# Performance work log

Measured on AMD Instinct MI355X. Metric: run time of the kernel, lower is better.

## Reference

```python
import jax, jax.numpy as jnp
import numpy as np

B, H, L, D = 8, 8, 2048, 64
FACTOR = 5


def _num_sel(length):
    return min(int(FACTOR * np.ceil(np.log(length))), length)


def setup_inputs() -> dict:
    key = jax.random.key(0)
    kq, kk, kv, ki = jax.random.split(key, 4)
    num_k = _num_sel(L)
    return {
        "q": jax.random.normal(kq, (B, H, L, D), dtype=jnp.float32),
        "k": jax.random.normal(kk, (B, H, L, D), dtype=jnp.float32),
        "v": jax.random.normal(kv, (B, H, L, D), dtype=jnp.float32),
        "random_index": jax.random.randint(ki, (L, num_k), 0, L, dtype=jnp.int32),
    }


def reference(q, k, v, random_index):
    b, h, q_len, d = q.shape
    k_len = k.shape[2]
    num_q = _num_sel(q_len)

    # --- random K sampling per query: k_s[b,h,i,j,:] = k[b,h,random_index[i,j],:]
    k_s = k[:, :, random_index, :]                      # (B,H,L,num_k,D)
    pre_attn = jnp.einsum('bhid,bhijd->bhij', q, k_s)   # (B,H,L,num_k)
    measure = pre_attn.max(-1) - pre_attn.sum(-1) / k_len  # (B,H,L)

    # --- top-k query selection (sorted=False in torch; order-insensitive math)
    _, idx = jax.lax.top_k(measure, num_q)              # (B,H,num_q)
    q_sel = jnp.take_along_axis(q, idx[..., None], axis=2)  # (B,H,num_q,D)

    # --- reduced attention over all keys
    attn = jnp.einsum('bhid,bhjd->bhij', q_sel, k) * (d ** -0.5)  # (B,H,num_q,k_len)

    # ProbMask: causal mask per selected query index (mask where j > idx[i])
    mask = jnp.arange(k_len)[None, None, None, :] > idx[..., None]
    attn = jnp.where(mask, -jnp.inf, attn)
    attn = jax.nn.softmax(attn, axis=-1)

    out_sel = jnp.einsum('bhij,bhjd->bhid', attn, v)    # (B,H,num_q,D)

    # --- context initialization (use_mask=True branch) and scatter back
    context = jnp.cumsum(v, axis=2)                     # (B,H,L,D)
    bi = jnp.arange(b)[:, None, None]
    hi = jnp.arange(h)[None, :, None]
    out = context.at[bi, hi, idx].set(out_sel)          # (B,H,L,D)
    return out, attn
```

## Files before the change

### kernel.cpp

```cpp
#include <hip/hip_runtime.h>
#include <float.h>
#include <math.h>

#define B_  8
#define H_  8
#define L_  2048
#define D_  64
#define NS  40
#define BH  (B_*H_)
#define SCALE 0.125f


__global__ __launch_bounds__(256) void measure_kernel(
    const float* __restrict__ q, const float* __restrict__ k,
    const int* __restrict__ ridx, float* __restrict__ measure)
{
    int wave = threadIdx.x >> 6, lane = threadIdx.x & 63;
    int b = blockIdx.x;
    int xcd = b & 7, s = b >> 3;
    int bh  = xcd + ((s >> 9) << 3);
    int i   = (s & 511) * 4 + wave;
    int qj  = lane >> 4;
    int d4  = lane & 15;

    int rs = ridx[i * NS + (lane < NS ? lane : NS - 1)];

    const float4* kb = (const float4*)(k + (size_t)bh * L_ * D_);
    float4 qq = ((const float4*)(q + ((size_t)bh * L_ + i) * D_))[d4];

    float mx = -FLT_MAX, sm = 0.f;
    #pragma unroll
    for (int p = 0; p < 10; ++p) {
        int j = p * 4 + qj;
        int r = __shfl(rs, j, 64);
        float4 kk = kb[(size_t)r * 16 + d4];
        float pp = qq.x*kk.x + qq.y*kk.y + qq.z*kk.z + qq.w*kk.w;
        pp += __shfl_xor(pp, 1, 64);
        pp += __shfl_xor(pp, 2, 64);
        pp += __shfl_xor(pp, 4, 64);
        pp += __shfl_xor(pp, 8, 64);
        mx = fmaxf(mx, pp);
        sm += pp;
    }
    mx = fmaxf(mx, __shfl_xor(mx, 16, 64));  sm += __shfl_xor(sm, 16, 64);
    mx = fmaxf(mx, __shfl_xor(mx, 32, 64));  sm += __shfl_xor(sm, 32, 64);
    if (lane == 0)
        measure[(size_t)bh * L_ + i] = mx - sm * (1.0f / (float)L_);
}

__global__ __launch_bounds__(256) void topk_kernel(
    const float* __restrict__ measure, int* __restrict__ idxOut)
{
    __shared__ float wv[4]; __shared__ int wi[4];
    __shared__ float bvS;   __shared__ int biS;
    int b = blockIdx.x;
    int bh = (b & 7) + ((b >> 3) << 3);
    int t = threadIdx.x;
    const float4* m4 = (const float4*)(measure + (size_t)bh * L_);
    float vals[8];
    float4 a = m4[t*2], bb = m4[t*2 + 1];
    vals[0]=a.x; vals[1]=a.y; vals[2]=a.z; vals[3]=a.w;
    vals[4]=bb.x; vals[5]=bb.y; vals[6]=bb.z; vals[7]=bb.w;

    float lv = -FLT_MAX; int li = t*8;
    #pragma unroll
    for (int e = 0; e < 8; ++e) if (vals[e] > lv) { lv = vals[e]; li = t*8 + e; }

    int lane = t & 63, w = t >> 6;
    for (int r = 0; r < NS; ++r) {
        float v = lv; int idx = li;
        #pragma unroll
        for (int off = 32; off; off >>= 1) {
            float ov = __shfl_xor(v, off, 64);
            int   oi = __shfl_xor(idx, off, 64);
            if (ov > v || (ov == v && oi < idx)) { v = ov; idx = oi; }
        }
        if (lane == 0) { wv[w] = v; wi[w] = idx; }
        __syncthreads();
        if (t == 0) {
            float bv = wv[0]; int bi = wi[0];
            #pragma unroll
            for (int ww = 1; ww < 4; ++ww)
                if (wv[ww] > bv || (wv[ww] == bv && wi[ww] < bi)) { bv = wv[ww]; bi = wi[ww]; }
            bvS = bv; biS = bi;
            idxOut[bh * NS + r] = bi;
        }
        __syncthreads();
        int bi = biS;
        if ((bi >> 3) == t) {
            #pragma unroll
            for (int e = 0; e < 8; ++e) if ((bi & 7) == e) vals[e] = -FLT_MAX;
            lv = -FLT_MAX; li = t*8;
            #pragma unroll
            for (int e = 0; e < 8; ++e) if (vals[e] > lv) { lv = vals[e]; li = t*8 + e; }
        }
        __syncthreads();
    }
}

__global__ __launch_bounds__(256) void cumsum_p1(
    const float* __restrict__ v, float4* __restrict__ vpart)
{
    __shared__ float4 part[16][16];
    int b = blockIdx.x;
    int xcd = b & 7, s = b >> 3;
    int bh = xcd + ((s >> 4) << 3);
    int c  = s & 15;
    int d4 = threadIdx.x & 15, sub = threadIdx.x >> 4;
    const float4* vb = (const float4*)(v + (size_t)bh * L_ * D_);
    int r0 = c*128 + sub*8;
    float4 acc = make_float4(0,0,0,0);
    #pragma unroll
    for (int r = 0; r < 8; ++r) {
        float4 x = vb[(r0 + r)*16 + d4];
        acc.x += x.x; acc.y += x.y; acc.z += x.z; acc.w += x.w;
    }
    part[sub][d4] = acc;
    __syncthreads();
    if (sub == 0) {
        float4 tot = part[0][d4];
        #pragma unroll
        for (int ss = 1; ss < 16; ++ss) {
            float4 x = part[ss][d4];
            tot.x += x.x; tot.y += x.y; tot.z += x.z; tot.w += x.w;
        }
        vpart[(bh*16 + c)*16 + d4] = tot;
    }
}

__global__ __launch_bounds__(256) void cumsum_p2(
    const float* __restrict__ v, const float4* __restrict__ vpart,
    float* __restrict__ out)
{
    __shared__ float4 part[16][16];
    int b = blockIdx.x;
    int xcd = b & 7, s = b >> 3;
    int bh = xcd + ((s >> 4) << 3);
    int c  = s & 15;
    int d4 = threadIdx.x & 15, sub = threadIdx.x >> 4;
    const float4* vb = (const float4*)(v + (size_t)bh * L_ * D_);
    float4*       ob = (float4*)(out + (size_t)bh * L_ * D_);
    int r0 = c*128 + sub*8;
    float4 acc = make_float4(0,0,0,0);
    #pragma unroll
    for (int r = 0; r < 8; ++r) {
        float4 x = vb[(r0 + r)*16 + d4];
        acc.x += x.x; acc.y += x.y; acc.z += x.z; acc.w += x.w;
    }
    part[sub][d4] = acc;
    float4 run = make_float4(0,0,0,0);
    for (int cc = 0; cc < c; ++cc) {
        float4 x = vpart[(bh*16 + cc)*16 + d4];
        run.x += x.x; run.y += x.y; run.z += x.z; run.w += x.w;
    }
    __syncthreads();
    #pragma unroll
    for (int ss = 0; ss < 16; ++ss) {
        if (ss < sub) {
            float4 x = part[ss][d4];
            run.x += x.x; run.y += x.y; run.z += x.z; run.w += x.w;
        }
    }
    #pragma unroll
    for (int r = 0; r < 8; ++r) {
        float4 x = vb[(r0 + r)*16 + d4];
        run.x += x.x; run.y += x.y; run.z += x.z; run.w += x.w;
        ob[(r0 + r)*16 + d4] = run;
    }
}

__global__ __launch_bounds__(256) void scores_kernel(
    const float* __restrict__ q, const float* __restrict__ k,
    const int* __restrict__ idxSel, float* __restrict__ attn)
{
    __shared__ float4 kbuf[16 * 129];
    int b = blockIdx.x;
    int xcd = b & 7, s = b >> 3;
    int bh  = xcd + ((s / 10) << 3);
    int grp = s % 10;
    int qi = threadIdx.x >> 6, sub = threadIdx.x & 63;
    int rank = grp*4 + qi;
    int qrow = idxSel[bh*NS + rank];

    const float4* qrp = (const float4*)(q + ((size_t)bh * L_ + qrow) * D_);
    float4 qreg[16];
    #pragma unroll
    for (int g = 0; g < 16; ++g) qreg[g] = qrp[g];

    const float4* kb = (const float4*)(k + (size_t)bh * L_ * D_);
    float sc0[16], sc1[16];

    #pragma unroll
    for (int c = 0; c < 16; ++c) {
        __syncthreads();
        int j0 = c * 128;
        #pragma unroll
        for (int it = 0; it < 8; ++it) {
            int fi = threadIdx.x + 256*it;
            int g = fi & 15, j = fi >> 4;
            kbuf[g*129 + j] = kb[(size_t)(j0 + j)*16 + g];
        }
        __syncthreads();
        float acc0 = 0.f, acc1 = 0.f;
        #pragma unroll
        for (int g = 0; g < 16; ++g) {
            float4 k0 = kbuf[g*129 + sub];
            float4 k1 = kbuf[g*129 + sub + 64];
            float4 qq = qreg[g];
            acc0 += qq.x*k0.x + qq.y*k0.y + qq.z*k0.z + qq.w*k0.w;
            acc1 += qq.x*k1.x + qq.y*k1.y + qq.z*k1.z + qq.w*k1.w;
        }
        sc0[c] = acc0 * SCALE;
        sc1[c] = acc1 * SCALE;
    }

    float mx = -FLT_MAX;
    #pragma unroll
    for (int c = 0; c < 16; ++c) {
        if (c*128 + sub      <= qrow) mx = fmaxf(mx, sc0[c]);
        if (c*128 + sub + 64 <= qrow) mx = fmaxf(mx, sc1[c]);
    }
    #pragma unroll
    for (int off = 32; off; off >>= 1) mx = fmaxf(mx, __shfl_xor(mx, off, 64));

    float sum = 0.f;
    #pragma unroll
    for (int c = 0; c < 16; ++c) {
        sc0[c] = (c*128 + sub      <= qrow) ? __expf(sc0[c] - mx) : 0.f;
        sc1[c] = (c*128 + sub + 64 <= qrow) ? __expf(sc1[c] - mx) : 0.f;
        sum += sc0[c] + sc1[c];
    }
    #pragma unroll
    for (int off = 32; off; off >>= 1) sum += __shfl_xor(sum, off, 64);
    float inv = 1.f / sum;

    float* arow = attn + (size_t)(bh*NS + rank) * L_;
    #pragma unroll
    for (int c = 0; c < 16; ++c) {
        arow[c*128 + sub]      = sc0[c] * inv;
        arow[c*128 + sub + 64] = sc1[c] * inv;
    }
}

__global__ __launch_bounds__(256) void pv_kernel(
    const float* __restrict__ v, const int* __restrict__ idxSel,
    const float* __restrict__ attn, float* __restrict__ out)
{
    __shared__ float wl[4][L_ + 64];
    __shared__ float4 part[16][16];
    __shared__ int qr4[4];
    int b = blockIdx.x;
    int xcd = b & 7, s = b >> 3;
    int bh  = xcd + ((s / 10) << 3);
    int grp = s % 10;
    int t = threadIdx.x;
    if (t < 4) qr4[t] = idxSel[bh*NS + grp*4 + t];

    #pragma unroll
    for (int it = 0; it < 8; ++it) {
        int f = t + 256*it;
        int rr = f >> 9, fi = f & 511;
        const float4* ar = (const float4*)(attn + (size_t)(bh*NS + grp*4 + rr) * L_);
        float4 x = ar[fi];
        int j = 4*fi;
        *((float4*)&wl[rr][j + 4*(j >> 7)]) = x;
    }
    __syncthreads();

    int maxq = max(max(qr4[0], qr4[1]), max(qr4[2], qr4[3]));
    int d4 = t & 15, seg = t >> 4;
    const float4* vb = (const float4*)(v + (size_t)bh * L_ * D_);
    float4 acc[4];
    #pragma unroll
    for (int rr = 0; rr < 4; ++rr) acc[rr] = make_float4(0,0,0,0);

    int jlo = seg*128, jhi = min(jlo + 127, maxq);
    for (int j = jlo; j <= jhi; ++j) {
        float4 x = vb[(size_t)j*16 + d4];
        int jp = j + 4*(j >> 7);
        #pragma unroll
        for (int rr = 0; rr < 4; ++rr) {
            float wgt = wl[rr][jp];
            acc[rr].x += wgt*x.x; acc[rr].y += wgt*x.y;
            acc[rr].z += wgt*x.z; acc[rr].w += wgt*x.w;
        }
    }

    #pragma unroll
    for (int rr = 0; rr < 4; ++rr) {
        part[seg][d4] = acc[rr];
        __syncthreads();
        float4 a = acc[rr];
        for (int s2 = 8; s2; s2 >>= 1) {
            if (seg < s2) {
                float4 o = part[seg + s2][d4];
                a.x += o.x; a.y += o.y; a.z += o.z; a.w += o.w;
                part[seg][d4] = a;
            }
            __syncthreads();
        }
        if (seg == 0) {
            float4* orow = (float4*)(out + ((size_t)bh * L_ + qr4[rr]) * D_);
            orow[d4] = a;
        }
        __syncthreads();
    }
}

extern "C" void kernel_launch(void* const* d_in, const int* in_sizes, int n_in,
                              void* d_out, int out_size, void* d_ws, size_t ws_size,
                              hipStream_t stream) {
    const float* q    = (const float*)d_in[0];
    const float* k    = (const float*)d_in[1];
    const float* v    = (const float*)d_in[2];
    const int*   ridx = (const int*)d_in[3];

    float* out     = (float*)d_out;
    float* attnOut = out + (size_t)BH * L_ * D_;

    float*  measure = (float*)d_ws;
    int*    idxSel  = (int*)((char*)d_ws + (size_t)BH * L_ * sizeof(float));
    float4* vpart   = (float4*)d_ws;

    measure_kernel<<<BH * L_ / 4, 256, 0, stream>>>(q, k, ridx, measure);
    topk_kernel   <<<BH,          256, 0, stream>>>(measure, idxSel);
    cumsum_p1     <<<BH * 16,     256, 0, stream>>>(v, vpart);
    cumsum_p2     <<<BH * 16,     256, 0, stream>>>(v, vpart, out);
    scores_kernel <<<BH * 10,     256, 0, stream>>>(q, k, idxSel, attnOut);
    pv_kernel     <<<BH * 10,     256, 0, stream>>>(v, idxSel, attnOut, out);
}
```

Measured before the change: 331.2 us.

## Merge six launches into three fused kernels with DPP reductions

Runs measure together with the cumsum partial pass in one launch, and top-k together with the cumsum final pass in a second. Scores and PV are fused so attention weights go straight into shared memory instead of being reloaded from global. The measure reduction now uses DPP moves in place of shuffles, and random indices are read directly rather than broadcast. Fewer launch gaps and less global traffic, but the fused scores/PV kernel uses more shared memory, which may lower occupancy.

```diff
diff --git a/kernel.cpp b/kernel.cpp
--- a/kernel.cpp
+++ b/kernel.cpp
@@ -11,169 +11,173 @@
 #define SCALE 0.125f
 
 
-__global__ __launch_bounds__(256) void measure_kernel(
+template<int CTRL>
+__device__ __forceinline__ float dpp_mov(float x) {
+    return __int_as_float(__builtin_amdgcn_update_dpp(
+        0, __float_as_int(x), CTRL, 0xf, 0xf, true));
+}
+
+__global__ __launch_bounds__(256) void kernelA(
     const float* __restrict__ q, const float* __restrict__ k,
-    const int* __restrict__ ridx, float* __restrict__ measure)
+    const int* __restrict__ ridx, const float* __restrict__ v,
+    float* __restrict__ measure, float4* __restrict__ vpart)
 {
-    int wave = threadIdx.x >> 6, lane = threadIdx.x & 63;
-    int b = blockIdx.x;
-    int xcd = b & 7, s = b >> 3;
-    int bh  = xcd + ((s >> 9) << 3);
-    int i   = (s & 511) * 4 + wave;
-    int qj  = lane >> 4;
-    int d4  = lane & 15;
-
-    int rs = ridx[i * NS + (lane < NS ? lane : NS - 1)];
-
-    const float4* kb = (const float4*)(k + (size_t)bh * L_ * D_);
-    float4 qq = ((const float4*)(q + ((size_t)bh * L_ + i) * D_))[d4];
-
-    float mx = -FLT_MAX, sm = 0.f;
-    #pragma unroll
-    for (int p = 0; p < 10; ++p) {
-        int j = p * 4 + qj;
-        int r = __shfl(rs, j, 64);
-        float4 kk = kb[(size_t)r * 16 + d4];
-        float pp = qq.x*kk.x + qq.y*kk.y + qq.z*kk.z + qq.w*kk.w;
-        pp += __shfl_xor(pp, 1, 64);
-        pp += __shfl_xor(pp, 2, 64);
-        pp += __shfl_xor(pp, 4, 64);
-        pp += __shfl_xor(pp, 8, 64);
-        mx = fmaxf(mx, pp);
-        sm += pp;
-    }
-    mx = fmaxf(mx, __shfl_xor(mx, 16, 64));  sm += __shfl_xor(sm, 16, 64);
-    mx = fmaxf(mx, __shfl_xor(mx, 32, 64));  sm += __shfl_xor(sm, 32, 64);
-    if (lane == 0)
-        measure[(size_t)bh * L_ + i] = mx - sm * (1.0f / (float)L_);
-}
-
-__global__ __launch_bounds__(256) void topk_kernel(
-    const float* __restrict__ measure, int* __restrict__ idxOut)
-{
-    __shared__ float wv[4]; __shared__ int wi[4];
-    __shared__ float bvS;   __shared__ int biS;
-    int b = blockIdx.x;
-    int bh = (b & 7) + ((b >> 3) << 3);
-    int t = threadIdx.x;
-    const float4* m4 = (const float4*)(measure + (size_t)bh * L_);
-    float vals[8];
-    float4 a = m4[t*2], bb = m4[t*2 + 1];
-    vals[0]=a.x; vals[1]=a.y; vals[2]=a.z; vals[3]=a.w;
-    vals[4]=bb.x; vals[5]=bb.y; vals[6]=bb.z; vals[7]=bb.w;
-
-    float lv = -FLT_MAX; int li = t*8;
-    #pragma unroll
-    for (int e = 0; e < 8; ++e) if (vals[e] > lv) { lv = vals[e]; li = t*8 + e; }
-
-    int lane = t & 63, w = t >> 6;
-    for (int r = 0; r < NS; ++r) {
-        float v = lv; int idx = li;
-        #pragma unroll
-        for (int off = 32; off; off >>= 1) {
-            float ov = __shfl_xor(v, off, 64);
-            int   oi = __shfl_xor(idx, off, 64);
-            if (ov > v || (ov == v && oi < idx)) { v = ov; idx = oi; }
-        }
-        if (lane == 0) { wv[w] = v; wi[w] = idx; }
-        __syncthreads();
-        if (t == 0) {
-            float bv = wv[0]; int bi = wi[0];
+    if (blockIdx.x < 32768) {
+        int wave = threadIdx.x >> 6, lane = threadIdx.x & 63;
+        int b = blockIdx.x;
+        int xcd = b & 7, s = b >> 3;
+        int bh  = xcd + ((s >> 9) << 3);
+        int i   = (s & 511) * 4 + wave;
+        int qj  = lane >> 4;
+        int d4  = lane & 15;
+
+        const float4* kb = (const float4*)(k + (size_t)bh * L_ * D_);
+        float4 qq = ((const float4*)(q + ((size_t)bh * L_ + i) * D_))[d4];
+        const int* rip = ridx + i * NS + qj;
+
+        float mx = -FLT_MAX, sm = 0.f;
+        #pragma unroll
+        for (int p = 0; p < 10; ++p) {
+            int r = rip[p * 4];
+            float4 kk = kb[(size_t)r * 16 + d4];
+            float pp = qq.x*kk.x + qq.y*kk.y + qq.z*kk.z + qq.w*kk.w;
+            pp += dpp_mov<0xB1>(pp);
+            pp += dpp_mov<0x4E>(pp);
+            pp += dpp_mov<0x124>(pp);
+            pp += dpp_mov<0x128>(pp);
+            mx = fmaxf(mx, pp);
+            sm += pp;
+        }
+        mx = fmaxf(mx, dpp_mov<0x142>(mx));  sm += dpp_mov<0x142>(sm);
+        mx = fmaxf(mx, dpp_mov<0x143>(mx));  sm += dpp_mov<0x143>(sm);
+        if (lane == 63)
+            measure[(size_t)bh * L_ + i] = mx - sm * (1.0f / (float)L_);
+    } else {
+        __shared__ float4 part[16][16];
+        int b = blockIdx.x - 32768;
+        int xcd = b & 7, s = b >> 3;
+        int bh = xcd + ((s >> 4) << 3);
+        int c  = s & 15;
+        int d4 = threadIdx.x & 15, sub = threadIdx.x >> 4;
+        const float4* vb = (const float4*)(v + (size_t)bh * L_ * D_);
+        int r0 = c*128 + sub*8;
+        float4 acc = make_float4(0,0,0,0);
+        #pragma unroll
+        for (int r = 0; r < 8; ++r) {
+            float4 x = vb[(r0 + r)*16 + d4];
+            acc.x += x.x; acc.y += x.y; acc.z += x.z; acc.w += x.w;
+        }
+        part[sub][d4] = acc;
+        __syncthreads();
+        if (sub == 0) {
+            float4 tot = part[0][d4];
             #pragma unroll
-            for (int ww = 1; ww < 4; ++ww)
-                if (wv[ww] > bv || (wv[ww] == bv && wi[ww] < bi)) { bv = wv[ww]; bi = wi[ww]; }
-            bvS = bv; biS = bi;
-            idxOut[bh * NS + r] = bi;
-        }
-        __syncthreads();
-        int bi = biS;
-        if ((bi >> 3) == t) {
-            #pragma unroll
-            for (int e = 0; e < 8; ++e) if ((bi & 7) == e) vals[e] = -FLT_MAX;
-            lv = -FLT_MAX; li = t*8;
-            #pragma unroll
-            for (int e = 0; e < 8; ++e) if (vals[e] > lv) { lv = vals[e]; li = t*8 + e; }
-        }
-        __syncthreads();
-    }
-}
-
-__global__ __launch_bounds__(256) void cumsum_p1(
-    const float* __restrict__ v, float4* __restrict__ vpart)
-{
-    __shared__ float4 part[16][16];
-    int b = blockIdx.x;
-    int xcd = b & 7, s = b >> 3;
-    int bh = xcd + ((s >> 4) << 3);
-    int c  = s & 15;
-    int d4 = threadIdx.x & 15, sub = threadIdx.x >> 4;
-    const float4* vb = (const float4*)(v + (size_t)bh * L_ * D_);
-    int r0 = c*128 + sub*8;
-    float4 acc = make_float4(0,0,0,0);
-    #pragma unroll
-    for (int r = 0; r < 8; ++r) {
-        float4 x = vb[(r0 + r)*16 + d4];
-        acc.x += x.x; acc.y += x.y; acc.z += x.z; acc.w += x.w;
-    }
-    part[sub][d4] = acc;
-    __syncthreads();
-    if (sub == 0) {
-        float4 tot = part[0][d4];
-        #pragma unroll
-        for (int ss = 1; ss < 16; ++ss) {
-            float4 x = part[ss][d4];
-            tot.x += x.x; tot.y += x.y; tot.z += x.z; tot.w += x.w;
-        }
-        vpart[(bh*16 + c)*16 + d4] = tot;
-    }
-}
-
-__global__ __launch_bounds__(256) void cumsum_p2(
-    const float* __restrict__ v, const float4* __restrict__ vpart,
+            for (int ss = 1; ss < 16; ++ss) {
+                float4 x = part[ss][d4];
+                tot.x += x.x; tot.y += x.y; tot.z += x.z; tot.w += x.w;
+            }
+            vpart[(bh*16 + c)*16 + d4] = tot;
+        }
+    }
+}
+
+__global__ __launch_bounds__(256) void kernelB(
+    const float* __restrict__ measure, const float* __restrict__ v,
+    const float4* __restrict__ vpart, int* __restrict__ idxOut,
     float* __restrict__ out)
 {
-    __shared__ float4 part[16][16];
-    int b = blockIdx.x;
-    int xcd = b & 7, s = b >> 3;
-    int bh = xcd + ((s >> 4) << 3);
-    int c  = s & 15;
-    int d4 = threadIdx.x & 15, sub = threadIdx.x >> 4;
-    const float4* vb = (const float4*)(v + (size_t)bh * L_ * D_);
-    float4*       ob = (float4*)(out + (size_t)bh * L_ * D_);
-    int r0 = c*128 + sub*8;
-    float4 acc = make_float4(0,0,0,0);
-    #pragma unroll
-    for (int r = 0; r < 8; ++r) {
-        float4 x = vb[(r0 + r)*16 + d4];
-        acc.x += x.x; acc.y += x.y; acc.z += x.z; acc.w += x.w;
-    }
-    part[sub][d4] = acc;
-    float4 run = make_float4(0,0,0,0);
-    for (int cc = 0; cc < c; ++cc) {
-        float4 x = vpart[(bh*16 + cc)*16 + d4];
-        run.x += x.x; run.y += x.y; run.z += x.z; run.w += x.w;
-    }
-    __syncthreads();
-    #pragma unroll
-    for (int ss = 0; ss < 16; ++ss) {
-        if (ss < sub) {
-            float4 x = part[ss][d4];
+    if (blockIdx.x < 64) {
+        __shared__ float wv[4]; __shared__ int wi[4];
+        __shared__ int biS;
+        int bh = blockIdx.x, t = threadIdx.x;
+        const float4* m4 = (const float4*)(measure + (size_t)bh * L_);
+        float vals[8];
+        float4 a = m4[t*2], bb = m4[t*2 + 1];
+        vals[0]=a.x; vals[1]=a.y; vals[2]=a.z; vals[3]=a.w;
+        vals[4]=bb.x; vals[5]=bb.y; vals[6]=bb.z; vals[7]=bb.w;
+
+        float lv = -FLT_MAX; int li = t*8;
+        #pragma unroll
+        for (int e = 0; e < 8; ++e) if (vals[e] > lv) { lv = vals[e]; li = t*8 + e; }
+
+        int lane = t & 63, w = t >> 6;
+        for (int r = 0; r < NS; ++r) {
+            float vv = lv; int idx = li;
+            #pragma unroll
+            for (int off = 32; off; off >>= 1) {
+                float ov = __shfl_xor(vv, off, 64);
+                int   oi = __shfl_xor(idx, off, 64);
+                if (ov > vv || (ov == vv && oi < idx)) { vv = ov; idx = oi; }
+            }
+            if (lane == 0) { wv[w] = vv; wi[w] = idx; }
+            __syncthreads();
+            if (t == 0) {
+                float bv = wv[0]; int bi = wi[0];
+                #pragma unroll
+                for (int ww = 1; ww < 4; ++ww)
+                    if (wv[ww] > bv || (wv[ww] == bv && wi[ww] < bi)) { bv = wv[ww]; bi = wi[ww]; }
+                biS = bi;
+                idxOut[bh * NS + r] = bi;
+            }
+            __syncthreads();
+            int bi = biS;
+            if ((bi >> 3) == t) {
+                #pragma unroll
+                for (int e = 0; e < 8; ++e) if ((bi & 7) == e) vals[e] = -FLT_MAX;
+                lv = -FLT_MAX; li = t*8;
+                #pragma unroll
+                for (int e = 0; e < 8; ++e) if (vals[e] > lv) { lv = vals[e]; li = t*8 + e; }
+            }
+            __syncthreads();
+        }
+    } else {
+        __shared__ float4 part[16][16];
+        int b = blockIdx.x - 64;
+        int xcd = b & 7, s = b >> 3;
+        int bh = xcd + ((s >> 4) << 3);
+        int c  = s & 15;
+        int d4 = threadIdx.x & 15, sub = threadIdx.x >> 4;
+        const float4* vb = (const float4*)(v + (size_t)bh * L_ * D_);
+        float4*       ob = (float4*)(out + (size_t)bh * L_ * D_);
+        int r0 = c*128 + sub*8;
+        float4 acc = make_float4(0,0,0,0);
+        #pragma unroll
+        for (int r = 0; r < 8; ++r) {
+            float4 x = vb[(r0 + r)*16 + d4];
+            acc.x += x.x; acc.y += x.y; acc.z += x.z; acc.w += x.w;
+        }
+        part[sub][d4] = acc;
+        float4 run = make_float4(0,0,0,0);
+        for (int cc = 0; cc < c; ++cc) {
+            float4 x = vpart[(bh*16 + cc)*16 + d4];
             run.x += x.x; run.y += x.y; run.z += x.z; run.w += x.w;
         }
-    }
-    #pragma unroll
-    for (int r = 0; r < 8; ++r) {
-        float4 x = vb[(r0 + r)*16 + d4];
-        run.x += x.x; run.y += x.y; run.z += x.z; run.w += x.w;
-        ob[(r0 + r)*16 + d4] = run;
-    }
-}
-
-__global__ __launch_bounds__(256) void scores_kernel(
+        __syncthreads();
+        #pragma unroll
+        for (int ss = 0; ss < 16; ++ss) {
+            if (ss < sub) {
+                float4 x = part[ss][d4];
+                run.x += x.x; run.y += x.y; run.z += x.z; run.w += x.w;
+            }
+        }
+        #pragma unroll
+        for (int r = 0; r < 8; ++r) {
+            float4 x = vb[(r0 + r)*16 + d4];
+            run.x += x.x; run.y += x.y; run.z += x.z; run.w += x.w;
+            ob[(r0 + r)*16 + d4] = run;
+        }
+    }
+}
+
+__global__ __launch_bounds__(256) void kernelC(
     const float* __restrict__ q, const float* __restrict__ k,
-    const int* __restrict__ idxSel, float* __restrict__ attn)
+    const float* __restrict__ v, const int* __restrict__ idxSel,
+    float* __restrict__ out, float* __restrict__ attn)
 {
     __shared__ float4 kbuf[16 * 129];
+    __shared__ float wl[4][L_ + 64];
+    __shared__ float4 part[16][16];
+    __shared__ int qr4[4];
     int b = blockIdx.x;
     int xcd = b & 7, s = b >> 3;
     int bh  = xcd + ((s / 10) << 3);
@@ -181,6 +185,7 @@
     int qi = threadIdx.x >> 6, sub = threadIdx.x & 63;
     int rank = grp*4 + qi;
     int qrow = idxSel[bh*NS + rank];
+    if (sub == 0) qr4[qi] = qrow;
 
     const float4* qrp = (const float4*)(q + ((size_t)bh * L_ + qrow) * D_);
     float4 qreg[16];
@@ -237,36 +242,16 @@
     float* arow = attn + (size_t)(bh*NS + rank) * L_;
     #pragma unroll
     for (int c = 0; c < 16; ++c) {
-        arow[c*128 + sub]      = sc0[c] * inv;
-        arow[c*128 + sub + 64] = sc1[c] * inv;
-    }
-}
-
-__global__ __launch_bounds__(256) void pv_kernel(
-    const float* __restrict__ v, const int* __restrict__ idxSel,
-    const float* __restrict__ attn, float* __restrict__ out)
-{
-    __shared__ float wl[4][L_ + 64];
-    __shared__ float4 part[16][16];
-    __shared__ int qr4[4];
-    int b = blockIdx.x;
-    int xcd = b & 7, s = b >> 3;
-    int bh  = xcd + ((s / 10) << 3);
-    int grp = s % 10;
+        float w0 = sc0[c] * inv, w1 = sc1[c] * inv;
+        int j0 = c*128 + sub, j1 = c*128 + sub + 64;
+        arow[j0] = w0;
+        arow[j1] = w1;
+        wl[qi][j0 + 4*(j0 >> 7)] = w0;
+        wl[qi][j1 + 4*(j1 >> 7)] = w1;
+    }
+    __syncthreads();
+
     int t = threadIdx.x;
-    if (t < 4) qr4[t] = idxSel[bh*NS + grp*4 + t];
-
-    #pragma unroll
-    for (int it = 0; it < 8; ++it) {
-        int f = t + 256*it;
-        int rr = f >> 9, fi = f & 511;
-        const float4* ar = (const float4*)(attn + (size_t)(bh*NS + grp*4 + rr) * L_);
-        float4 x = ar[fi];
-        int j = 4*fi;
-        *((float4*)&wl[rr][j + 4*(j >> 7)]) = x;
-    }
-    __syncthreads();
-
     int maxq = max(max(qr4[0], qr4[1]), max(qr4[2], qr4[3]));
     int d4 = t & 15, seg = t >> 4;
     const float4* vb = (const float4*)(v + (size_t)bh * L_ * D_);
@@ -319,13 +304,10 @@
     float* attnOut = out + (size_t)BH * L_ * D_;
 
     float*  measure = (float*)d_ws;
-    int*    idxSel  = (int*)((char*)d_ws + (size_t)BH * L_ * sizeof(float));
-    float4* vpart   = (float4*)d_ws;
-
-    measure_kernel<<<BH * L_ / 4, 256, 0, stream>>>(q, k, ridx, measure);
-    topk_kernel   <<<BH,          256, 0, stream>>>(measure, idxSel);
-    cumsum_p1     <<<BH * 16,     256, 0, stream>>>(v, vpart);
-    cumsum_p2     <<<BH * 16,     256, 0, stream>>>(v, vpart, out);
-    scores_kernel <<<BH * 10,     256, 0, stream>>>(q, k, idxSel, attnOut);
-    pv_kernel     <<<BH * 10,     256, 0, stream>>>(v, idxSel, attnOut, out);
-}
+    float4* vpart   = (float4*)((char*)d_ws + 524288);
+    int*    idxSel  = (int*)((char*)d_ws + 524288 + 262144);
+
+    kernelA<<<32768 + 1024, 256, 0, stream>>>(q, k, ridx, v, measure, vpart);
+    kernelB<<<64 + 1024,    256, 0, stream>>>(measure, v, vpart, idxSel, out);
+    kernelC<<<BH * 10,      256, 0, stream>>>(q, k, v, idxSel, out, attnOut);
+}
```

Result: slower. 342.2 us (+3.3%).
